# Optimization experiments

Measured on AMD Instinct MI355X. Metric: run time of the kernel, lower is better.

## Reference

```python
import jax, jax.numpy as jnp
import numpy as np

D_MODEL = 2048
D_FF = 8192


def absmean_quant(w):
    # scale = mean(|w|); keep weights whose magnitude >= 0.7*scale, ternarize to {-1,0,1}
    scale = jnp.mean(jnp.abs(w))
    mask = (jnp.abs(w) >= scale * 0.7).astype(w.dtype)
    return jnp.sign(w) * mask


def setup_inputs() -> dict:
    key = jax.random.key(0)
    k_x, k_w1, k_w2 = jax.random.split(key, 3)
    x = jax.random.normal(k_x, (4, 4096, D_MODEL), dtype=jnp.float32)
    w1 = jax.random.normal(k_w1, (D_FF, D_MODEL), dtype=jnp.float32)  # fc1.weight
    b1 = jnp.zeros((D_FF,), dtype=jnp.float32)
    w2 = jax.random.normal(k_w2, (D_MODEL, D_FF), dtype=jnp.float32)  # fc2.weight
    b2 = jnp.zeros((D_MODEL,), dtype=jnp.float32)
    return {"x": x, "w1": w1, "b1": b1, "w2": w2, "b2": b2}


def reference(x, w1, b1, w2, b2):
    w1_q = absmean_quant(w1)
    w2_q = absmean_quant(w2)
    h = jnp.einsum('bsd,fd->bsf', x, w1_q) + b1  # fc1: [B,S,d_ff]
    h = jax.nn.gelu(h, approximate=False)        # torch nn.GELU default = exact erf
    out = jnp.einsum('bsf,df->bsd', h, w2_q) + b2  # fc2: [B,S,d_model]
    return out
```

## Files before the change

kernel.cpp:

```cpp
#include <hip/hip_runtime.h>
#include <hip/hip_bf16.h>
#include <math.h>
#include <stdint.h>

#define D_MODEL 2048
#define D_FF    8192
#define MTOK    16384
#define NW      (D_FF * D_MODEL)

typedef int    i32x4  __attribute__((ext_vector_type(4)));
typedef __bf16 bf16x8 __attribute__((ext_vector_type(8)));

#define GLOAD_LDS16(gp, lp)                                                   \
  __builtin_amdgcn_global_load_lds(                                           \
      (__attribute__((address_space(1))) void*)(gp),                          \
      (__attribute__((address_space(3))) void*)(lp), 16, 0, 0)

__global__ void absum_s1(const float* __restrict__ w1, const float* __restrict__ w2,
                         double* __restrict__ partials) {
    const float* w = blockIdx.y ? w2 : w1;
    __shared__ double sm[256];
    int tid = blockIdx.x * 256 + threadIdx.x;
    double s = 0.0;
    for (int i = tid; i < NW / 4; i += 1024 * 256) {
        float4 v = ((const float4*)w)[i];
        s += (double)fabsf(v.x) + (double)fabsf(v.y) + (double)fabsf(v.z) + (double)fabsf(v.w);
    }
    sm[threadIdx.x] = s;
    __syncthreads();
    for (int off = 128; off > 0; off >>= 1) {
        if (threadIdx.x < off) sm[threadIdx.x] += sm[threadIdx.x + off];
        __syncthreads();
    }
    if (threadIdx.x == 0) partials[blockIdx.y * 1024 + blockIdx.x] = sm[0];
}

__global__ void absum_s2(const double* __restrict__ partials, float* __restrict__ thr) {
    __shared__ double sm[256];
    for (int wsel = 0; wsel < 2; ++wsel) {
        const double* p = partials + wsel * 1024;
        double s = p[threadIdx.x] + p[threadIdx.x + 256] + p[threadIdx.x + 512] + p[threadIdx.x + 768];
        sm[threadIdx.x] = s;
        __syncthreads();
        for (int off = 128; off > 0; off >>= 1) {
            if (threadIdx.x < off) sm[threadIdx.x] += sm[threadIdx.x + off];
            __syncthreads();
        }
        if (threadIdx.x == 0) thr[wsel] = (float)(0.7 * (sm[0] / (double)NW));
        __syncthreads();
    }
}

__global__ void quantw1(const float* __restrict__ w, const float* __restrict__ thr,
                        int8_t* __restrict__ q) {
    float t = thr[0];
    int i = (blockIdx.x * 256 + threadIdx.x) * 4;
    float4 v = *(const float4*)(w + i);
    char4 o;
    o.x = (fabsf(v.x) >= t) ? (v.x > 0.f ? 1 : -1) : 0;
    o.y = (fabsf(v.y) >= t) ? (v.y > 0.f ? 1 : -1) : 0;
    o.z = (fabsf(v.z) >= t) ? (v.z > 0.f ? 1 : -1) : 0;
    o.w = (fabsf(v.w) >= t) ? (v.w > 0.f ? 1 : -1) : 0;
    *(char4*)(q + i) = o;
}

__global__ void quantw2(const float* __restrict__ w, const float* __restrict__ thr,
                        int8_t* __restrict__ q, float* __restrict__ colsum) {
    __shared__ int sm[256];
    float t = thr[1];
    const int row = blockIdx.x;
    const int tid = threadIdx.x;
    int isum = 0;
    #pragma unroll
    for (int j = 0; j < 8; ++j) {
        int idx = row * D_FF + j * 1024 + tid * 4;
        float4 v = *(const float4*)(w + idx);
        char4 o;
        o.x = (fabsf(v.x) >= t) ? (v.x > 0.f ? 1 : -1) : 0;
        o.y = (fabsf(v.y) >= t) ? (v.y > 0.f ? 1 : -1) : 0;
        o.z = (fabsf(v.z) >= t) ? (v.z > 0.f ? 1 : -1) : 0;
        o.w = (fabsf(v.w) >= t) ? (v.w > 0.f ? 1 : -1) : 0;
        isum += o.x + o.y + o.z + o.w;
        *(char4*)(q + idx) = o;
    }
    sm[tid] = isum;
    __syncthreads();
    for (int off = 128; off > 0; off >>= 1) {
        if (tid < off) sm[tid] += sm[tid + off];
        __syncthreads();
    }
    if (tid == 0) colsum[row] = (float)sm[0];
}

__global__ void xquant(const float* __restrict__ x, int8_t* __restrict__ xq,
                       float* __restrict__ sx) {
    __shared__ float sm[256];
    const int row = blockIdx.x;
    const int tid = threadIdx.x;
    float4 v[2];
    float mx = 0.f;
    #pragma unroll
    for (int j = 0; j < 2; ++j) {
        v[j] = *(const float4*)(x + (size_t)row * D_MODEL + j * 1024 + tid * 4);
        mx = fmaxf(mx, fmaxf(fmaxf(fabsf(v[j].x), fabsf(v[j].y)),
                             fmaxf(fabsf(v[j].z), fabsf(v[j].w))));
    }
    sm[tid] = mx;
    __syncthreads();
    for (int off = 128; off > 0; off >>= 1) {
        if (tid < off) sm[tid] = fmaxf(sm[tid], sm[tid + off]);
        __syncthreads();
    }
    float m = sm[0];
    float inv = (m > 0.f) ? 127.f / m : 0.f;
    if (tid == 0) sx[row] = (m > 0.f) ? m / 127.f : 0.f;
    #pragma unroll
    for (int j = 0; j < 2; ++j) {
        char4 o;
        o.x = (int8_t)min(127, max(-127, __float2int_rn(v[j].x * inv)));
        o.y = (int8_t)min(127, max(-127, __float2int_rn(v[j].y * inv)));
        o.z = (int8_t)min(127, max(-127, __float2int_rn(v[j].z * inv)));
        o.w = (int8_t)min(127, max(-127, __float2int_rn(v[j].w * inv)));
        *(char4*)(xq + (size_t)row * D_MODEL + j * 1024 + tid * 4) = o;
    }
}

__global__ void hquant(const __bf16* __restrict__ h, int8_t* __restrict__ hq,
                       float2* __restrict__ sh) {
    __shared__ float sm[256];
    const int row = blockIdx.x;
    const int tid = threadIdx.x;
    const float gmin = -0.17f;
    float vals[4][8];
    float mx = -1e30f;
    #pragma unroll
    for (int j = 0; j < 4; ++j) {
        bf16x8 b = *(const bf16x8*)(h + (size_t)row * D_FF + j * 2048 + tid * 8);
        #pragma unroll
        for (int e = 0; e < 8; ++e) {
            float f = (float)b[e];
            vals[j][e] = f;
            mx = fmaxf(mx, f);
        }
    }
    sm[tid] = mx;
    __syncthreads();
    for (int off = 128; off > 0; off >>= 1) {
        if (tid < off) sm[tid] = fmaxf(sm[tid], sm[tid + off]);
        __syncthreads();
    }
    float M = sm[0];
    float s = (M - gmin) / 254.f;
    float inv = 254.f / (M - gmin);
    if (tid == 0) sh[row] = make_float2(s, 127.f * s + gmin);
    #pragma unroll
    for (int j = 0; j < 4; ++j) {
        char4 o0, o1;
        int q[8];
        #pragma unroll
        for (int e = 0; e < 8; ++e)
            q[e] = min(127, max(-127, __float2int_rn((vals[j][e] - gmin) * inv) - 127));
        o0.x = q[0]; o0.y = q[1]; o0.z = q[2]; o0.w = q[3];
        o1.x = q[4]; o1.y = q[5]; o1.z = q[6]; o1.w = q[7];
        int8_t* p = hq + (size_t)row * D_FF + j * 2048 + tid * 8;
        *(char4*)p = o0;
        *(char4*)(p + 4) = o1;
    }
}

template<int EPI>
__global__ __launch_bounds__(512, 4) void gemm_i8_bt(
    const int8_t* __restrict__ A,
    const int8_t* __restrict__ B,
    const float*  __restrict__ bias,
    const float*  __restrict__ rs,
    const float*  __restrict__ colsum,
    void* __restrict__ Cout,
    int M, int N, int K)
{
    __shared__ int8_t Sh[3 * 24576];

    const int tid  = threadIdx.x;
    const int wave = tid >> 6;
    const int lane = tid & 63;
    const int quad = lane >> 4;
    const int l15  = lane & 15;
    const int wm   = (wave >> 1) * 64;
    const int wn   = (wave & 1) * 64;

    const int gx   = gridDim.x;
    const int nwg  = gx * gridDim.y;
    const int orig = blockIdx.y * gx + blockIdx.x;
    int by, bx;
    if (EPI == 0) {
        const int swz = (orig & 7) * (nwg >> 3) + (orig >> 3);
        by = swz >> 6;
        bx = swz & 63;
    } else {
        const int xcd = orig & 7;
        const int l   = orig >> 3;
        const int st  = l >> 6;
        const int r   = l & 63;
        by = xcd * 8 + st * 4 + (r & 3);
        bx = r >> 2;
    }
    const int m0 = by << 8;
    const int n0 = bx << 7;

    i32x4 acc[4][4] = {};

    const int row0 = tid >> 2;
    const int cg0  = (tid & 3) ^ ((row0 >> 1) & 3);
    const int8_t* gA0 = A + (size_t)(m0 + row0) * K + cg0 * 16;
    const int8_t* gA1 = gA0 + (size_t)128 * K;
    const int8_t* gB0 = B + (size_t)(n0 + row0) * K + cg0 * 16;
    char* const ldsb = (char*)Sh;
    char* const dA0  = ldsb + wave * 1024;
    char* const dA1  = ldsb + 8192  + wave * 1024;
    char* const dB0  = ldsb + 16384 + wave * 1024;

    int aoff[4], boff[4];
    #pragma unroll
    for (int f = 0; f < 4; ++f) {
        int ra = wm + f * 16 + l15;
        aoff[f] = ra * 64 + ((quad ^ ((ra >> 1) & 3)) << 4);
        int rb = wn + f * 16 + l15;
        boff[f] = 16384 + rb * 64 + ((quad ^ ((rb >> 1) & 3)) << 4);
    }

    const int NH = K >> 6;
    const int STG = 24576;

    #pragma unroll
    for (int h = 0; h < 2; ++h) {
        GLOAD_LDS16(gA0, dA0 + h * STG);
        GLOAD_LDS16(gA1, dA1 + h * STG);
        GLOAD_LDS16(gB0, dB0 + h * STG);
        gA0 += 64; gA1 += 64; gB0 += 64;
    }
    asm volatile("s_waitcnt vmcnt(3)" ::: "memory");
    __builtin_amdgcn_s_barrier();
    __builtin_amdgcn_sched_barrier(0);

    int roff = 0;
    int soff = 2 * STG;

    for (int s = 0; s < NH; ++s) {
        if (s + 2 < NH) {
            GLOAD_LDS16(gA0, ldsb + soff + (dA0 - ldsb));
            GLOAD_LDS16(gA1, ldsb + soff + (dA1 - ldsb));
            GLOAD_LDS16(gB0, ldsb + soff + (dB0 - ldsb));
            gA0 += 64; gA1 += 64; gB0 += 64;
        }
        i32x4 bfr[4];
        #pragma unroll
        for (int f = 0; f < 4; ++f) bfr[f] = *(const i32x4*)(ldsb + roff + boff[f]);
        __builtin_amdgcn_s_setprio(1);
        #pragma unroll
        for (int mf = 0; mf < 4; ++mf) {
            i32x4 af = *(const i32x4*)(ldsb + roff + aoff[mf]);
            #pragma unroll
            for (int nf = 0; nf < 4; ++nf)
                acc[mf][nf] = __builtin_amdgcn_mfma_i32_16x16x64_i8(
                    af, bfr[nf], acc[mf][nf], 0, 0, 0);
        }
        __builtin_amdgcn_s_setprio(0);
        if (s < NH - 2)       { asm volatile("s_waitcnt vmcnt(3)" ::: "memory"); }
        else if (s == NH - 2) { asm volatile("s_waitcnt vmcnt(0)" ::: "memory"); }
        __builtin_amdgcn_sched_barrier(0);
        __builtin_amdgcn_s_barrier();
        __builtin_amdgcn_sched_barrier(0);
        roff = (roff == 2 * STG) ? 0 : roff + STG;
        soff = (soff == 2 * STG) ? 0 : soff + STG;
    }

    #pragma unroll
    for (int nf = 0; nf < 4; ++nf) {
        const int n = n0 + wn + nf * 16 + l15;
        const float bv = bias[n];
        const float cs = (EPI == 1) ? colsum[n] : 0.f;
        #pragma unroll
        for (int mf = 0; mf < 4; ++mf)
            #pragma unroll
            for (int r = 0; r < 4; ++r) {
                int m = m0 + wm + mf * 16 + quad * 4 + r;
                float a = (float)acc[mf][nf][r];
                if (EPI == 0) {
                    float v = rs[m] * a + bv;
                    v = 0.5f * v * (1.0f + erff(v * 0.70710678118654752f));
                    ((__bf16*)Cout)[(size_t)m * N + n] = (__bf16)v;
                } else {
                    float2 so = ((const float2*)rs)[m];
                    ((float*)Cout)[(size_t)m * N + n] = so.x * a + so.y * cs + bv;
                }
            }
    }
}

extern "C" void kernel_launch(void* const* d_in, const int* in_sizes, int n_in,
                              void* d_out, int out_size, void* d_ws, size_t ws_size,
                              hipStream_t stream) {
    const float* x  = (const float*)d_in[0];
    const float* w1 = (const float*)d_in[1];
    const float* b1 = (const float*)d_in[2];
    const float* w2 = (const float*)d_in[3];
    const float* b2 = (const float*)d_in[4];
    float* out = (float*)d_out;

    char* ws = (char*)d_ws;
    float*  thr = (float*)ws;
    float*  sx  = (float*)(ws + 256);
    float2* sh  = (float2*)(ws + 256 + (64 << 10));
    float*  colsum = (float*)(ws + 256 + (192 << 10));
    int8_t* xq  = (int8_t*)(ws + 256 + (256 << 10));
    int8_t* w1q = xq  + (size_t)MTOK * D_MODEL;
    int8_t* w2q = w1q + (size_t)D_FF * D_MODEL;
    int8_t* hq  = w2q + (size_t)D_MODEL * D_FF;
    __bf16* h   = (__bf16*)(hq + (size_t)MTOK * D_FF);
    double* partials = (double*)h;

    absum_s1<<<dim3(1024, 2), 256, 0, stream>>>(w1, w2, partials);
    absum_s2<<<1, 256, 0, stream>>>(partials, thr);

    quantw1<<<NW / 1024, 256, 0, stream>>>(w1, thr, w1q);
    quantw2<<<D_MODEL, 256, 0, stream>>>(w2, thr, w2q, colsum);
    xquant<<<MTOK, 256, 0, stream>>>(x, xq, sx);

    dim3 g1(D_FF / 128, MTOK / 256);
    gemm_i8_bt<0><<<g1, 512, 0, stream>>>(xq, w1q, b1, sx, nullptr, (void*)h,
                                          MTOK, D_FF, D_MODEL);

    hquant<<<MTOK, 256, 0, stream>>>(h, hq, sh);

    dim3 g2(D_MODEL / 128, MTOK / 256);
    gemm_i8_bt<1><<<g2, 512, 0, stream>>>(hq, w2q, b2, (const float*)sh, colsum, (void*)out,
                                          MTOK, D_MODEL, D_FF);
}
```

Before: 1.115 ms.

## Use 4 waves with 128x64 per-wave tiles in int8 GEMMs

The int8 GEMM block shrinks from 512 to 256 threads, and each wave now computes a 128x64 output tile with 8x4 MFMA accumulators instead of 64x64. Each thread issues more global-to-LDS loads per stage, and the wait counts are adjusted to match. The point is better register-level reuse of A/B fragments per LDS read and less barrier overhead per MFMA. In exchange it doubles accumulator registers, which can lower occupancy or cause spills. The fc1 GEMM also moves to the XCD-aware block swizzle that fc2 already used.

Result: slower. 1.138 ms (+2.1%).

```diff
diff --git a/kernel.cpp b/kernel.cpp
--- a/kernel.cpp
+++ b/kernel.cpp
@@ -169,7 +169,7 @@
 }
 
 template<int EPI>
-__global__ __launch_bounds__(512, 4) void gemm_i8_bt(
+__global__ __launch_bounds__(256, 2) void gemm_i8_bt(
     const int8_t* __restrict__ A,
     const int8_t* __restrict__ B,
     const float*  __restrict__ bias,
@@ -185,45 +185,53 @@
     const int lane = tid & 63;
     const int quad = lane >> 4;
     const int l15  = lane & 15;
-    const int wm   = (wave >> 1) * 64;
+    const int wm   = (wave >> 1) * 128;
     const int wn   = (wave & 1) * 64;
 
     const int gx   = gridDim.x;
-    const int nwg  = gx * gridDim.y;
     const int orig = blockIdx.y * gx + blockIdx.x;
-    int by, bx;
-    if (EPI == 0) {
-        const int swz = (orig & 7) * (nwg >> 3) + (orig >> 3);
-        by = swz >> 6;
-        bx = swz & 63;
-    } else {
-        const int xcd = orig & 7;
-        const int l   = orig >> 3;
-        const int st  = l >> 6;
-        const int r   = l & 63;
-        by = xcd * 8 + st * 4 + (r & 3);
-        bx = r >> 2;
-    }
+    const int xcd  = orig & 7;
+    const int l    = orig >> 3;
+    const int stsh = (EPI == 0) ? 8 : 6;
+    const int st   = l >> stsh;
+    const int r    = l & ((1 << stsh) - 1);
+    const int by   = xcd * 8 + st * 4 + (r & 3);
+    const int bx   = r >> 2;
     const int m0 = by << 8;
     const int n0 = bx << 7;
 
-    i32x4 acc[4][4] = {};
-
-    const int row0 = tid >> 2;
-    const int cg0  = (tid & 3) ^ ((row0 >> 1) & 3);
-    const int8_t* gA0 = A + (size_t)(m0 + row0) * K + cg0 * 16;
-    const int8_t* gA1 = gA0 + (size_t)128 * K;
-    const int8_t* gB0 = B + (size_t)(n0 + row0) * K + cg0 * 16;
+    i32x4 acc[8][4] = {};
+
+    const int8_t* gA[4]; const int8_t* gB[2];
+    #pragma unroll
+    for (int it = 0; it < 4; ++it) {
+        int slot = it * 256 + tid;
+        int row  = slot >> 2;
+        int cg   = (slot & 3) ^ ((row >> 1) & 3);
+        gA[it] = A + (size_t)(m0 + row) * K + cg * 16;
+    }
+    #pragma unroll
+    for (int it = 0; it < 2; ++it) {
+        int slot = it * 256 + tid;
+        int row  = slot >> 2;
+        int cg   = (slot & 3) ^ ((row >> 1) & 3);
+        gB[it] = B + (size_t)(n0 + row) * K + cg * 16;
+    }
     char* const ldsb = (char*)Sh;
-    char* const dA0  = ldsb + wave * 1024;
-    char* const dA1  = ldsb + 8192  + wave * 1024;
-    char* const dB0  = ldsb + 16384 + wave * 1024;
-
-    int aoff[4], boff[4];
-    #pragma unroll
-    for (int f = 0; f < 4; ++f) {
+    char* dA[4]; char* dB[2];
+    #pragma unroll
+    for (int it = 0; it < 4; ++it) dA[it] = ldsb + it * 4096 + wave * 1024;
+    #pragma unroll
+    for (int it = 0; it < 2; ++it) dB[it] = ldsb + 16384 + it * 4096 + wave * 1024;
+
+    int aoff[8], boff[4];
+    #pragma unroll
+    for (int f = 0; f < 8; ++f) {
         int ra = wm + f * 16 + l15;
         aoff[f] = ra * 64 + ((quad ^ ((ra >> 1) & 3)) << 4);
+    }
+    #pragma unroll
+    for (int f = 0; f < 4; ++f) {
         int rb = wn + f * 16 + l15;
         boff[f] = 16384 + rb * 64 + ((quad ^ ((rb >> 1) & 3)) << 4);
     }
@@ -233,12 +241,12 @@
 
     #pragma unroll
     for (int h = 0; h < 2; ++h) {
-        GLOAD_LDS16(gA0, dA0 + h * STG);
-        GLOAD_LDS16(gA1, dA1 + h * STG);
-        GLOAD_LDS16(gB0, dB0 + h * STG);
-        gA0 += 64; gA1 += 64; gB0 += 64;
-    }
-    asm volatile("s_waitcnt vmcnt(3)" ::: "memory");
+        #pragma unroll
+        for (int it = 0; it < 4; ++it) { GLOAD_LDS16(gA[it], dA[it] + h * STG); gA[it] += 64; }
+        #pragma unroll
+        for (int it = 0; it < 2; ++it) { GLOAD_LDS16(gB[it], dB[it] + h * STG); gB[it] += 64; }
+    }
+    asm volatile("s_waitcnt vmcnt(6)" ::: "memory");
     __builtin_amdgcn_s_barrier();
     __builtin_amdgcn_sched_barrier(0);
 
@@ -247,25 +255,25 @@
 
     for (int s = 0; s < NH; ++s) {
         if (s + 2 < NH) {
-            GLOAD_LDS16(gA0, ldsb + soff + (dA0 - ldsb));
-            GLOAD_LDS16(gA1, ldsb + soff + (dA1 - ldsb));
-            GLOAD_LDS16(gB0, ldsb + soff + (dB0 - ldsb));
-            gA0 += 64; gA1 += 64; gB0 += 64;
+            #pragma unroll
+            for (int it = 0; it < 4; ++it) { GLOAD_LDS16(gA[it], dA[it] + soff); gA[it] += 64; }
+            #pragma unroll
+            for (int it = 0; it < 2; ++it) { GLOAD_LDS16(gB[it], dB[it] + soff); gB[it] += 64; }
         }
-        i32x4 bfr[4];
+        i32x4 bfr[4], afr[8];
         #pragma unroll
         for (int f = 0; f < 4; ++f) bfr[f] = *(const i32x4*)(ldsb + roff + boff[f]);
+        #pragma unroll
+        for (int f = 0; f < 8; ++f) afr[f] = *(const i32x4*)(ldsb + roff + aoff[f]);
         __builtin_amdgcn_s_setprio(1);
         #pragma unroll
-        for (int mf = 0; mf < 4; ++mf) {
-            i32x4 af = *(const i32x4*)(ldsb + roff + aoff[mf]);
+        for (int mf = 0; mf < 8; ++mf)
             #pragma unroll
             for (int nf = 0; nf < 4; ++nf)
                 acc[mf][nf] = __builtin_amdgcn_mfma_i32_16x16x64_i8(
-                    af, bfr[nf], acc[mf][nf], 0, 0, 0);
-        }
+                    afr[mf], bfr[nf], acc[mf][nf], 0, 0, 0);
         __builtin_amdgcn_s_setprio(0);
-        if (s < NH - 2)       { asm volatile("s_waitcnt vmcnt(3)" ::: "memory"); }
+        if (s < NH - 2)       { asm volatile("s_waitcnt vmcnt(6)" ::: "memory"); }
         else if (s == NH - 2) { asm volatile("s_waitcnt vmcnt(0)" ::: "memory"); }
         __builtin_amdgcn_sched_barrier(0);
         __builtin_amdgcn_s_barrier();
@@ -280,7 +288,7 @@
         const float bv = bias[n];
         const float cs = (EPI == 1) ? colsum[n] : 0.f;
         #pragma unroll
-        for (int mf = 0; mf < 4; ++mf)
+        for (int mf = 0; mf < 8; ++mf)
             #pragma unroll
             for (int r = 0; r < 4; ++r) {
                 int m = m0 + wm + mf * 16 + quad * 4 + r;
@@ -327,12 +335,12 @@
     xquant<<<MTOK, 256, 0, stream>>>(x, xq, sx);
 
     dim3 g1(D_FF / 128, MTOK / 256);
-    gemm_i8_bt<0><<<g1, 512, 0, stream>>>(xq, w1q, b1, sx, nullptr, (void*)h,
+    gemm_i8_bt<0><<<g1, 256, 0, stream>>>(xq, w1q, b1, sx, nullptr, (void*)h,
                                           MTOK, D_FF, D_MODEL);
 
     hquant<<<MTOK, 256, 0, stream>>>(h, hq, sh);
 
     dim3 g2(D_MODEL / 128, MTOK / 256);
-    gemm_i8_bt<1><<<g2, 512, 0, stream>>>(hq, w2q, b2, (const float*)sh, colsum, (void*)out,
+    gemm_i8_bt<1><<<g2, 256, 0, stream>>>(hq, w2q, b2, (const float*)sh, colsum, (void*)out,
                                           MTOK, D_MODEL, D_FF);
 }
```
